# Optimization experiments

Measured on AMD Instinct MI355X. Metric: run time of the kernel, lower is better.

The kernel has to match this reference:

```python
import jax, jax.numpy as jnp
import numpy as np

TEMPERATURE = 0.1
EPS = 1e-8  # torch cosine_similarity eps
NEG_FILL = -9e15

def setup_inputs() -> dict:
    key = jax.random.key(0)
    stacked_batch = jax.random.normal(key, (8192, 128), dtype=jnp.float32)
    return {"stacked_batch": stacked_batch}

def reference(stacked_batch) -> jnp.ndarray:
    n = stacked_batch.shape[0]
    # cosine similarity = normalized GEMM (equivalent to torch broadcast form)
    norm = jnp.maximum(jnp.linalg.norm(stacked_batch, axis=-1, keepdims=True), EPS)
    z = stacked_batch / norm                      # [N, D]
    sim = jnp.matmul(z, z.T) / TEMPERATURE        # [N, N]
    # mask self-similarity on the diagonal
    idx = jnp.arange(n)
    sim = sim.at[idx, idx].set(NEG_FILL)
    # positive pair for row i is column (i + N/2) mod N
    pos_cols = (idx + n // 2) % n
    pos = sim[idx, pos_cols]                      # [N]
    loss = jax.scipy.special.logsumexp(sim, axis=-1) - pos
    return loss.mean()
```

## Files before the change

kernel.cpp:

```cpp
#include <hip/hip_runtime.h>
#include <hip/hip_bf16.h>

#define N 8192
#define D 128
#define HALF_N 4096
#define SQRT_SCALE_LOG2E 3.79828236f
#define LN2 0.693147180559945f

#define BLOCK_ROWS 256
#define COLS_PER_ITER 64
#define COL_SPLITS 16
#define COLS_PER_BLOCK (N / COL_SPLITS)
#define ITERS (COLS_PER_BLOCK / COLS_PER_ITER)
#define LDS_STRIDE 136

typedef short frag8 __attribute__((ext_vector_type(8)));
typedef float f32x4 __attribute__((ext_vector_type(4)));

#define OFF_POS    0
#define OFF_PSUMS  (N)
#define OFF_ACC    (N + COL_SPLITS * N)
#define OFF_Z_BYTES ((OFF_ACC + 64) * 4)

__device__ __forceinline__ unsigned short f2bf(float f) {
    unsigned int u = __float_as_uint(f);
    u += 0x7FFFu + ((u >> 16) & 1u);
    return (unsigned short)(u >> 16);
}

__global__ __launch_bounds__(256) void k_normalize(const float* __restrict__ x,
                                                   unsigned short* __restrict__ z,
                                                   float* __restrict__ acc0) {
    const int row  = blockIdx.x * 4 + (threadIdx.x >> 6);
    const int lane = threadIdx.x & 63;
    float2 v = ((const float2*)x)[row * 64 + lane];
    float s = v.x * v.x + v.y * v.y;
    #pragma unroll
    for (int m = 32; m >= 1; m >>= 1) s += __shfl_xor(s, m);
    float inv = SQRT_SCALE_LOG2E / fmaxf(sqrtf(s), 1e-8f);
    ushort2 o;
    o.x = f2bf(v.x * inv);
    o.y = f2bf(v.y * inv);
    ((ushort2*)z)[row * 64 + lane] = o;
    if (blockIdx.x == 0 && threadIdx.x == 0) acc0[0] = 0.0f;
}

__global__ __launch_bounds__(256, 2) void k_simloss(const unsigned short* __restrict__ z,
                                                    float* __restrict__ psums,
                                                    float* __restrict__ pos) {
    __shared__ unsigned short lds[COLS_PER_ITER * LDS_STRIDE];

    const int tid  = threadIdx.x;
    const int wave = tid >> 6;
    const int lane = tid & 63;
    const int l15  = lane & 15;
    const int quad = lane >> 4;
    const int wrow = blockIdx.x * BLOCK_ROWS + wave * 64;
    const int colbase0 = blockIdx.y * COLS_PER_BLOCK;
    const int posbase  = (wrow + HALF_N) & (N - 1);

    frag8 a[4][4];
    #pragma unroll
    for (int s = 0; s < 4; ++s) {
        const uint4* p = (const uint4*)&z[(wrow + s * 16 + l15) * D + quad * 8];
        #pragma unroll
        for (int q = 0; q < 4; ++q) {
            uint4 t = p[q * 4];
            a[s][q] = *(frag8*)&t;
        }
    }

    float sums[4][4];
    #pragma unroll
    for (int s = 0; s < 4; ++s)
        #pragma unroll
        for (int r = 0; r < 4; ++r) sums[s][r] = 0.0f;

    for (int it = 0; it < ITERS; ++it) {
        const int colbase = colbase0 + it * COLS_PER_ITER;
        __syncthreads();
        #pragma unroll
        for (int u = 0; u < 4; ++u) {
            int idx = u * 256 + tid;
            int r   = idx >> 4;
            int c8  = idx & 15;
            uint4 t = *(const uint4*)&z[(colbase + r) * D + c8 * 8];
            *(uint4*)&lds[r * LDS_STRIDE + c8 * 8] = t;
        }
        __syncthreads();

        const bool isDiag = (colbase == wrow);
        const bool isPos  = (colbase == posbase);
        const unsigned short* lp = &lds[l15 * LDS_STRIDE + quad * 8];

        #pragma unroll
        for (int c = 0; c < 4; ++c) {
            f32x4 acc[4];
            #pragma unroll
            for (int s = 0; s < 4; ++s) acc[s] = (f32x4){0.f, 0.f, 0.f, 0.f};
            #pragma unroll
            for (int q = 0; q < 4; ++q) {
                frag8 b = *(const frag8*)(lp + c * 16 * LDS_STRIDE + q * 32);
                #pragma unroll
                for (int s = 0; s < 4; ++s)
                    acc[s] = __builtin_amdgcn_mfma_f32_16x16x32_bf16(a[s][q], b, acc[s], 0, 0, 0);
            }
            if (isDiag | isPos) {
                #pragma unroll
                for (int s = 0; s < 4; ++s)
                    #pragma unroll
                    for (int r = 0; r < 4; ++r) {
                        float v = acc[s][r];
                        float e = __builtin_amdgcn_exp2f(v);
                        if (c == s) {
                            bool hit = (l15 == quad * 4 + r);
                            if (isDiag && hit) e = 0.0f;
                            if (isPos  && hit) pos[wrow + s * 16 + quad * 4 + r] = v * LN2;
                        }
                        sums[s][r] += e;
                    }
            } else {
                #pragma unroll
                for (int s = 0; s < 4; ++s)
                    #pragma unroll
                    for (int r = 0; r < 4; ++r)
                        sums[s][r] += __builtin_amdgcn_exp2f(acc[s][r]);
            }
        }
    }

    #pragma unroll
    for (int s = 0; s < 4; ++s)
        #pragma unroll
        for (int r = 0; r < 4; ++r) {
            float v = sums[s][r];
            v += __shfl_xor(v, 1);
            v += __shfl_xor(v, 2);
            v += __shfl_xor(v, 4);
            v += __shfl_xor(v, 8);
            if (l15 == 0)
                psums[blockIdx.y * N + wrow + s * 16 + quad * 4 + r] = v;
        }
}

__global__ __launch_bounds__(1024) void k_rowloss(const float* __restrict__ psums,
                                                  const float* __restrict__ pos,
                                                  float* __restrict__ acc0) {
    const int row = blockIdx.x * 1024 + threadIdx.x;
    float t = 0.0f;
    #pragma unroll
    for (int s = 0; s < COL_SPLITS; ++s) t += psums[s * N + row];
    float loss = __logf(t) - pos[row];
    #pragma unroll
    for (int m = 32; m >= 1; m >>= 1) loss += __shfl_xor(loss, m);
    __shared__ float p[16];
    if ((threadIdx.x & 63) == 0) p[threadIdx.x >> 6] = loss;
    __syncthreads();
    if (threadIdx.x == 0) {
        float s = 0.0f;
        #pragma unroll
        for (int w = 0; w < 16; ++w) s += p[w];
        atomicAdd(acc0, s);
    }
}

__global__ void k_final(const float* __restrict__ acc0, float* __restrict__ out) {
    out[0] = acc0[0] * (1.0f / N);
}

extern "C" void kernel_launch(void* const* d_in, const int* in_sizes, int n_in,
                              void* d_out, int out_size, void* d_ws, size_t ws_size,
                              hipStream_t stream) {
    const float* x = (const float*)d_in[0];
    float* wsf   = (float*)d_ws;
    float* pos   = wsf + OFF_POS;
    float* psums = wsf + OFF_PSUMS;
    float* acc0  = wsf + OFF_ACC;
    unsigned short* z = (unsigned short*)((char*)d_ws + OFF_Z_BYTES);

    k_normalize<<<N / 4, 256, 0, stream>>>(x, z, acc0);
    dim3 g2(N / BLOCK_ROWS, COL_SPLITS);
    k_simloss<<<g2, 256, 0, stream>>>(z, psums, pos);
    k_rowloss<<<N / 1024, 1024, 0, stream>>>(psums, pos, acc0);
    k_final<<<1, 1, 0, stream>>>(acc0, (float*)d_out);
}
```

Measured before the change: 84.01 us.

## Prefetch next column tile into registers and fuse final reduction via completion counter

The similarity kernel now loads the next 64-column tile from global memory into registers while the current tile's MFMAs run, overlapping global latency with compute at the cost of 16 extra VGPRs per thread. The final scalar kernel is removed: the row-loss kernel uses 256-thread blocks and a last-block-done atomic counter to write the mean directly, saving one launch. The counter is reset in the normalize kernel.

Result: slower. 90.95 us (+8.3%).

```diff
diff --git a/kernel.cpp b/kernel.cpp
--- a/kernel.cpp
+++ b/kernel.cpp
@@ -20,6 +20,7 @@
 #define OFF_POS    0
 #define OFF_PSUMS  (N)
 #define OFF_ACC    (N + COL_SPLITS * N)
+#define OFF_CNT    (OFF_ACC + 1)
 #define OFF_Z_BYTES ((OFF_ACC + 64) * 4)
 
 __device__ __forceinline__ unsigned short f2bf(float f) {
@@ -30,7 +31,8 @@
 
 __global__ __launch_bounds__(256) void k_normalize(const float* __restrict__ x,
                                                    unsigned short* __restrict__ z,
-                                                   float* __restrict__ acc0) {
+                                                   float* __restrict__ acc0,
+                                                   unsigned int* __restrict__ counter) {
     const int row  = blockIdx.x * 4 + (threadIdx.x >> 6);
     const int lane = threadIdx.x & 63;
     float2 v = ((const float2*)x)[row * 64 + lane];
@@ -42,7 +44,7 @@
     o.x = f2bf(v.x * inv);
     o.y = f2bf(v.y * inv);
     ((ushort2*)z)[row * 64 + lane] = o;
-    if (blockIdx.x == 0 && threadIdx.x == 0) acc0[0] = 0.0f;
+    if (blockIdx.x == 0 && threadIdx.x == 0) { acc0[0] = 0.0f; counter[0] = 0u; }
 }
 
 __global__ __launch_bounds__(256, 2) void k_simloss(const unsigned short* __restrict__ z,
@@ -58,6 +60,9 @@
     const int wrow = blockIdx.x * BLOCK_ROWS + wave * 64;
     const int colbase0 = blockIdx.y * COLS_PER_BLOCK;
     const int posbase  = (wrow + HALF_N) & (N - 1);
+
+    const int st_r  = tid >> 4;
+    const int st_c8 = tid & 15;
 
     frag8 a[4][4];
     #pragma unroll
@@ -76,18 +81,25 @@
         #pragma unroll
         for (int r = 0; r < 4; ++r) sums[s][r] = 0.0f;
 
+    uint4 t[4];
+    #pragma unroll
+    for (int u = 0; u < 4; ++u)
+        t[u] = *(const uint4*)&z[(colbase0 + u * 16 + st_r) * D + st_c8 * 8];
+
     for (int it = 0; it < ITERS; ++it) {
         const int colbase = colbase0 + it * COLS_PER_ITER;
         __syncthreads();
         #pragma unroll
-        for (int u = 0; u < 4; ++u) {
-            int idx = u * 256 + tid;
-            int r   = idx >> 4;
-            int c8  = idx & 15;
-            uint4 t = *(const uint4*)&z[(colbase + r) * D + c8 * 8];
-            *(uint4*)&lds[r * LDS_STRIDE + c8 * 8] = t;
+        for (int u = 0; u < 4; ++u)
+            *(uint4*)&lds[(u * 16 + st_r) * LDS_STRIDE + st_c8 * 8] = t[u];
+        __syncthreads();
+
+        if (it + 1 < ITERS) {
+            const int nb = colbase + COLS_PER_ITER;
+            #pragma unroll
+            for (int u = 0; u < 4; ++u)
+                t[u] = *(const uint4*)&z[(nb + u * 16 + st_r) * D + st_c8 * 8];
         }
-        __syncthreads();
 
         const bool isDiag = (colbase == wrow);
         const bool isPos  = (colbase == posbase);
@@ -143,29 +155,30 @@
         }
 }
 
-__global__ __launch_bounds__(1024) void k_rowloss(const float* __restrict__ psums,
-                                                  const float* __restrict__ pos,
-                                                  float* __restrict__ acc0) {
-    const int row = blockIdx.x * 1024 + threadIdx.x;
+__global__ __launch_bounds__(256) void k_rowloss(const float* __restrict__ psums,
+                                                 const float* __restrict__ pos,
+                                                 float* __restrict__ acc0,
+                                                 unsigned int* __restrict__ counter,
+                                                 float* __restrict__ out) {
+    const int row = blockIdx.x * 256 + threadIdx.x;
     float t = 0.0f;
     #pragma unroll
     for (int s = 0; s < COL_SPLITS; ++s) t += psums[s * N + row];
     float loss = __logf(t) - pos[row];
     #pragma unroll
     for (int m = 32; m >= 1; m >>= 1) loss += __shfl_xor(loss, m);
-    __shared__ float p[16];
+    __shared__ float p[4];
     if ((threadIdx.x & 63) == 0) p[threadIdx.x >> 6] = loss;
     __syncthreads();
     if (threadIdx.x == 0) {
-        float s = 0.0f;
-        #pragma unroll
-        for (int w = 0; w < 16; ++w) s += p[w];
-        atomicAdd(acc0, s);
+        atomicAdd(acc0, p[0] + p[1] + p[2] + p[3]);
+        __threadfence();
+        unsigned prev = atomicAdd(counter, 1u);
+        if (prev == gridDim.x - 1) {
+            float total = atomicAdd(acc0, 0.0f);
+            out[0] = total * (1.0f / N);
+        }
     }
-}
-
-__global__ void k_final(const float* __restrict__ acc0, float* __restrict__ out) {
-    out[0] = acc0[0] * (1.0f / N);
 }
 
 extern "C" void kernel_launch(void* const* d_in, const int* in_sizes, int n_in,
@@ -176,11 +189,11 @@
     float* pos   = wsf + OFF_POS;
     float* psums = wsf + OFF_PSUMS;
     float* acc0  = wsf + OFF_ACC;
+    unsigned int* counter = (unsigned int*)(wsf + OFF_CNT);
     unsigned short* z = (unsigned short*)((char*)d_ws + OFF_Z_BYTES);
 
-    k_normalize<<<N / 4, 256, 0, stream>>>(x, z, acc0);
+    k_normalize<<<N / 4, 256, 0, stream>>>(x, z, acc0, counter);
     dim3 g2(N / BLOCK_ROWS, COL_SPLITS);
     k_simloss<<<g2, 256, 0, stream>>>(z, psums, pos);
-    k_rowloss<<<N / 1024, 1024, 0, stream>>>(psums, pos, acc0);
-    k_final<<<1, 1, 0, stream>>>(acc0, (float*)d_out);
+    k_rowloss<<<N / 256, 256, 0, stream>>>(psums, pos, acc0, counter, (float*)d_out);
 }
```
